# Optimization experiments

Hardware: AMD Instinct MI355X
Metric: run time of the kernel (lower is better)

## Reference

```python
import jax, jax.numpy as jnp
import numpy as np

CTX = 2048
D_IN = 2048
D_OUT = 2048
N_HEADS = 16
HEAD_DIM = D_OUT // N_HEADS
ROPE_BASE = 10000.0


def rope_tables(head_dim, ctx):
    inv_freq = 1.0 / (ROPE_BASE ** (jnp.arange(0, head_dim, 2, dtype=jnp.float32) / head_dim))
    angles = jnp.arange(ctx, dtype=jnp.float32)[:, None] * inv_freq[None, :]  # [ctx, hd/2]
    angles = jnp.concatenate([angles, angles], axis=1)  # [ctx, hd]
    return jnp.sin(angles), jnp.cos(angles)


def apply_rope(x, sin, cos):
    # x: [b, h, s, d]; rotate-by-half (Raschka / Llama style)
    s = x.shape[2]
    d = x.shape[3]
    x1, x2 = x[..., : d // 2], x[..., d // 2 :]
    rotated = jnp.concatenate([-x2, x1], axis=-1)
    return x * cos[:s][None, None] + rotated * sin[:s][None, None]


def setup_inputs() -> dict:
    key = jax.random.key(0)
    kx, kq, kk, kv, ko = jax.random.split(key, 5)
    scale = 0.02
    return {
        "x": jax.random.normal(kx, (2, CTX, D_IN), dtype=jnp.float32),
        "W_query": jax.random.normal(kq, (D_IN, D_OUT), dtype=jnp.float32) * scale,
        "W_key": jax.random.normal(kk, (D_IN, D_OUT), dtype=jnp.float32) * scale,
        "W_value": jax.random.normal(kv, (D_IN, D_OUT), dtype=jnp.float32) * scale,
        "W_out": jax.random.normal(ko, (D_OUT, D_OUT), dtype=jnp.float32) * scale,
    }


def reference(x, W_query, W_key, W_value, W_out):
    bs, cl, _ = x.shape
    sin, cos = rope_tables(HEAD_DIM, CTX)

    def split_heads(t):  # [b, s, d_out] -> [b, h, s, hd]
        return t.reshape(bs, cl, N_HEADS, HEAD_DIM).transpose(0, 2, 1, 3)

    q = split_heads(x @ W_query)
    k = split_heads(x @ W_key)
    v = split_heads(x @ W_value)

    q = apply_rope(q, sin, cos)
    k = apply_rope(k, sin, cos)

    # NOTE: original module does NOT scale by 1/sqrt(head_dim)
    scores = jnp.einsum("bhqd,bhkd->bhqk", q, k)
    causal = jnp.triu(jnp.ones((cl, cl), dtype=bool), k=1)
    scores = jnp.where(causal[None, None], -jnp.inf, scores)
    weights = jax.nn.softmax(scores, axis=-1)
    ctx = jnp.einsum("bhqk,bhkd->bhqd", weights, v)
    ctx = ctx.transpose(0, 2, 1, 3).reshape(bs, cl, N_HEADS * HEAD_DIM)
    return ctx @ W_out
```

## Files before the change

kernel.cpp:

```cpp
#include <hip/hip_runtime.h>
#include <cstdint>
#include <cstddef>

typedef _Float16 f16;
typedef _Float16 f16x8 __attribute__((ext_vector_type(8)));
typedef _Float16 f16x4 __attribute__((ext_vector_type(4)));
typedef float    f32x4 __attribute__((ext_vector_type(4)));
typedef float    f32x16 __attribute__((ext_vector_type(16)));
typedef int      i32x4 __attribute__((ext_vector_type(4)));

#define S_CTX 2048
#define NH 16
#define DH 128

#define BAR() asm volatile("s_barrier" ::: "memory")
#define VMW(n) asm volatile("s_waitcnt vmcnt(" #n ")" ::: "memory")
#define MF(a, b, c) __builtin_amdgcn_mfma_f32_16x16x32_f16((a), (b), (c), 0, 0, 0)
#define MF32(a, b, c) __builtin_amdgcn_mfma_f32_32x32x16_f16((a), (b), (c), 0, 0, 0)

__device__ __forceinline__ void gload16(const void* g, void* l) {
  __builtin_amdgcn_global_load_lds(
      (const __attribute__((address_space(1))) void*)g,
      (__attribute__((address_space(3))) void*)l, 16, 0, 0);
}

__device__ __forceinline__ int pk2(float a, float b) {
  auto hv = __builtin_amdgcn_cvt_pkrtz(a, b);
  return __builtin_bit_cast(int, hv);
}
__device__ __forceinline__ void pl_swap(int& a, int& b) {
  asm volatile("v_permlane32_swap_b32 %0, %1" : "+v"(a), "+v"(b));
}

__global__ void prep(const float* __restrict__ x,
                     const float* __restrict__ w0, const float* __restrict__ w1,
                     const float* __restrict__ w2, const float* __restrict__ w3,
                     f16* __restrict__ xb,
                     f16* __restrict__ o0, f16* __restrict__ o1,
                     f16* __restrict__ o2, f16* __restrict__ o3,
                     float* __restrict__ sint, float* __restrict__ cost) {
  const int bid = blockIdx.x, tid = threadIdx.x;
  if (bid < 512) {
    int idx = bid * 256 + tid;
    int j = idx & 63, s = idx >> 6;
    float invf = __expf(-(float)(2 * j) * (1.0f / 128.0f) * 9.210340371976184f);
    float a = (float)s * invf;
    sint[idx] = sinf(a);
    cost[idx] = cosf(a);
  } else if (bid < 8704) {
    int i = ((bid - 512) * 256 + tid) * 4;
    float4 v = *(const float4*)(x + i);
    f16x4 o; o[0] = (f16)v.x; o[1] = (f16)v.y; o[2] = (f16)v.z; o[3] = (f16)v.w;
    *(f16x4*)(xb + i) = o;
  } else {
    int b2 = bid - 8704;
    int z = b2 >> 12, rem = b2 & 4095;
    int by = rem >> 6, bx = rem & 63;
    int tx = tid & 31, ty = tid >> 5;
    const float* in; f16* out;
    switch (z) {
      case 0: in = w0; out = o0; break;
      case 1: in = w1; out = o1; break;
      case 2: in = w2; out = o2; break;
      default: in = w3; out = o3; break;
    }
    __shared__ float tl[32][33];
    int xc = bx * 32 + tx, yc = by * 32 + ty;
#pragma unroll
    for (int r = 0; r < 32; r += 8)
      tl[ty + r][tx] = in[(size_t)(yc + r) * 2048 + xc];
    __syncthreads();
    int xo = by * 32 + tx, yo = bx * 32 + ty;
#pragma unroll
    for (int r = 0; r < 32; r += 8)
      out[(size_t)(yo + r) * 2048 + xo] = (f16)tl[tx][ty + r];
  }
}

__global__ __launch_bounds__(512, 1)
void gemm_qk(const f16* __restrict__ A, const f16* __restrict__ wqT,
             const f16* __restrict__ wkT,
             f16* __restrict__ qb, f16* __restrict__ kb,
             const float* __restrict__ sint, const float* __restrict__ cost) {
  extern __shared__ __align__(16) char lds[];
  const int tid = threadIdx.x, lane = tid & 63;
  const int wvi = tid >> 6, wm = wvi >> 2, wn = wvi & 3;
  const int gcol = blockIdx.x * 256;
  const int proj = gcol >> 11;
  const int col0 = gcol & 2047;
  const int row0 = blockIdx.y * 256;
  const f16* Bt = proj ? wkT : wqT;

  const int ca0 = tid, ca1 = tid + 512;
  const int ra0 = ca0 >> 2, ra1 = ca1 >> 2;
  const int sa0 = (ca0 & 3) ^ ((ra0 >> 1) & 3);
  const int sa1 = (ca1 & 3) ^ ((ra1 >> 1) & 3);
  const f16* gA0 = A + (size_t)(row0 + ra0) * 2048 + sa0 * 8;
  const f16* gA1 = A + (size_t)(row0 + ra1) * 2048 + sa1 * 8;
  const f16* gB0 = Bt + (size_t)(col0 + ra0) * 2048 + sa0 * 8;
  const f16* gB1 = Bt + (size_t)(col0 + ra1) * 2048 + sa1 * 8;

  const int kslot = lane >> 4;
  int aoff[8], boff[4];
#pragma unroll
  for (int i = 0; i < 8; i++) {
    int row = wm * 128 + i * 16 + (lane & 15);
    aoff[i] = row * 64 + ((kslot ^ ((row >> 1) & 3)) << 4);
  }
#pragma unroll
  for (int j = 0; j < 4; j++) {
    int rb = (wn >> 1) * 128 + (wn & 1) * 32 + (j & 1) * 16 + (j >> 1) * 64 + (lane & 15);
    boff[j] = rb * 64 + ((kslot ^ ((rb >> 1) & 3)) << 4);
  }

  f32x4 acc[8][4] = {};

#define QKPH(SLOT, HS, SSLOT, DOSTAGE, WN) do {                                \
    const char* As_ = lds + (SLOT) * 32768;                                    \
    const char* Bs_ = As_ + 16384;                                             \
    f16x8 af[8], bf[4];                                                        \
    _Pragma("unroll") for (int i_ = 0; i_ < 8; i_++)                           \
      af[i_] = *(const f16x8*)(As_ + aoff[i_]);                                \
    _Pragma("unroll") for (int j_ = 0; j_ < 4; j_++)                           \
      bf[j_] = *(const f16x8*)(Bs_ + boff[j_]);                                \
    if (DOSTAGE) {                                                             \
      char* dA = lds + (SSLOT) * 32768;                                        \
      gload16(gA0 + (HS) * 32, dA + ca0 * 16);                                 \
      gload16(gA1 + (HS) * 32, dA + ca1 * 16);                                 \
      gload16(gB0 + (HS) * 32, dA + 16384 + ca0 * 16);                         \
      gload16(gB1 + (HS) * 32, dA + 16384 + ca1 * 16);                         \
    }                                                                          \
    asm volatile("s_waitcnt vmcnt(" #WN ")" ::: "memory");                     \
    BAR();                                                                     \
    __builtin_amdgcn_s_setprio(1);                                             \
    _Pragma("unroll") for (int i_ = 0; i_ < 8; i_++)                           \
      _Pragma("unroll") for (int j_ = 0; j_ < 4; j_++)                         \
        acc[i_][j_] = MF(af[i_], bf[j_], acc[i_][j_]);                         \
    __builtin_amdgcn_s_setprio(0);                                             \
    BAR();                                                                     \
  } while (0)

#pragma unroll
  for (int h = 0; h < 2; h++) {
    char* dA = lds + h * 32768;
    gload16(gA0 + h * 32, dA + ca0 * 16);
    gload16(gA1 + h * 32, dA + ca1 * 16);
    gload16(gB0 + h * 32, dA + 16384 + ca0 * 16);
    gload16(gB1 + h * 32, dA + 16384 + ca1 * 16);
  }
  VMW(4); BAR();

  for (int t = 0; t < 20; ++t) {
    const int hb = 3 * t;
    QKPH(0, hb + 2, 2, 1, 4);
    QKPH(1, hb + 3, 0, 1, 4);
    QKPH(2, hb + 4, 1, 1, 4);
  }
  QKPH(0, 62, 2, 1, 4);
  QKPH(1, 63, 0, 1, 4);
  QKPH(2, 0, 0, 0, 0);
  QKPH(0, 0, 0, 0, 63);
#undef QKPH

  const int b = row0 >> 11, sb = row0 & 2047;
  f16* dst = proj ? kb : qb;
  const int h = (col0 >> 7) + (wn >> 1);
#pragma unroll
  for (int i = 0; i < 8; i++)
#pragma unroll
    for (int jj = 0; jj < 2; jj++)
#pragma unroll
      for (int r = 0; r < 4; r++) {
        int s = sb + wm * 128 + i * 16 + (lane >> 4) * 4 + r;
        int d = (wn & 1) * 32 + jj * 16 + (lane & 15);
        float cv = cost[s * 64 + d], sv = sint[s * 64 + d];
        float x1 = acc[i][jj][r], x2 = acc[i][jj + 2][r];
        size_t base = ((size_t)(b * NH + h) * S_CTX + s) << 7;
        dst[base + d]      = (f16)(x1 * cv - x2 * sv);
        dst[base + d + 64] = (f16)(x2 * cv + x1 * sv);
      }
}

template<int MODE>
__global__ __launch_bounds__(512, 1)
void gemm8(const f16* __restrict__ A, const f16* __restrict__ Bt,
           f16* __restrict__ vtb, float* __restrict__ of) {
  extern __shared__ __align__(16) char lds[];
#define RING_A(e) (lds + (e) * 16384)
#define RING_B(e) (lds + 65536 + (e) * 8192)
  const int tid = threadIdx.x, lane = tid & 63;
  const int wvi = tid >> 6, wm = wvi >> 1, wn = wvi & 1;
  const int col0 = blockIdx.x * 128;
  const int row0 = blockIdx.y * 256;

  const int ca0 = tid, ca1 = tid + 512, cb0 = tid;
  const int rAs0 = ca0 >> 2, rAs1 = ca1 >> 2, rBs0 = cb0 >> 2;
  const int sA0 = (ca0 & 3) ^ ((rAs0 >> 1) & 3);
  const int sA1 = (ca1 & 3) ^ ((rAs1 >> 1) & 3);
  const int sB0 = (cb0 & 3) ^ ((rBs0 >> 1) & 3);
  const f16* gA0 = A + (size_t)(row0 + rAs0) * 2048 + sA0 * 8;
  const f16* gA1 = A + (size_t)(row0 + rAs1) * 2048 + sA1 * 8;
  const f16* gB0 = Bt + (size_t)(col0 + rBs0) * 2048 + sB0 * 8;

  const int kslot = lane >> 4;
  int aoff[4], boff[4];
#pragma unroll
  for (int i = 0; i < 4; i++) {
    int row = wm * 64 + i * 16 + (lane & 15);
    aoff[i] = row * 64 + ((kslot ^ ((row >> 1) & 3)) << 4);
  }
#pragma unroll
  for (int j = 0; j < 4; j++) {
    int rb = wn * 32 + (j & 1) * 16 + (j >> 1) * 64 + (lane & 15);
    boff[j] = rb * 64 + ((kslot ^ ((rb >> 1) & 3)) << 4);
  }

  f32x4 acc[4][4] = {};

#define PH8(SLOT, HS, DOSTAGE, WN) do {                                        \
    const char* As_ = RING_A(SLOT);                                            \
    const char* Bs_ = RING_B(SLOT);                                            \
    f16x8 af[4], bf[4];                                                        \
    _Pragma("unroll") for (int i_ = 0; i_ < 4; i_++)                           \
      af[i_] = *(const f16x8*)(As_ + aoff[i_]);                                \
    _Pragma("unroll") for (int j_ = 0; j_ < 4; j_++)                           \
      bf[j_] = *(const f16x8*)(Bs_ + boff[j_]);                                \
    if (DOSTAGE) {                                                             \
      gload16(gA0 + (HS) * 32, RING_A((HS) & 3) + ca0 * 16);                   \
      gload16(gA1 + (HS) * 32, RING_A((HS) & 3) + ca1 * 16);                   \
      gload16(gB0 + (HS) * 32, RING_B((HS) & 3) + cb0 * 16);                   \
    }                                                                          \
    asm volatile("s_waitcnt vmcnt(" #WN ")" ::: "memory");                     \
    BAR();                                                                     \
    __builtin_amdgcn_s_setprio(1);                                             \
    _Pragma("unroll") for (int i_ = 0; i_ < 4; i_++)                           \
      _Pragma("unroll") for (int j_ = 0; j_ < 4; j_++)                         \
        acc[i_][j_] = MF(af[i_], bf[j_], acc[i_][j_]);                         \
    __builtin_amdgcn_s_setprio(0);                                             \
    BAR();                                                                     \
  } while (0)

#pragma unroll
  for (int h = 0; h < 3; h++) {
    gload16(gA0 + h * 32, RING_A(h) + ca0 * 16);
    gload16(gA1 + h * 32, RING_A(h) + ca1 * 16);
    gload16(gB0 + h * 32, RING_B(h) + cb0 * 16);
  }
  VMW(6); BAR();

  for (int t = 0; t < 15; ++t) {
    const int p = t * 4;
    PH8(0, p + 3, 1, 6);
    PH8(1, p + 4, 1, 6);
    PH8(2, p + 5, 1, 6);
    PH8(3, p + 6, 1, 6);
  }
  PH8(0, 63, 1, 6);
  PH8(1, 0, 0, 3);
  PH8(2, 0, 0, 0);
  PH8(3, 0, 0, 63);
#undef PH8

  const int b = row0 >> 11, sbase = row0 & 2047;

  if (MODE == 2) {
#pragma unroll
    for (int i = 0; i < 4; i++)
#pragma unroll
      for (int j = 0; j < 4; j++)
#pragma unroll
        for (int r = 0; r < 4; r++) {
          int row = row0 + wm * 64 + i * 16 + (lane >> 4) * 4 + r;
          int col = col0 + wn * 32 + (j & 1) * 16 + (j >> 1) * 64 + (lane & 15);
          of[(size_t)row * 2048 + col] = acc[i][j][r];
        }
  } else {
    const int h = col0 >> 7;
    f16x4* ldsv = (f16x4*)lds;
#pragma unroll
    for (int i = 0; i < 4; i++)
#pragma unroll
      for (int j = 0; j < 4; j++) {
        f16x4 v;
#pragma unroll
        for (int r = 0; r < 4; r++) v[r] = (f16)acc[i][j][r];
        int su = wm * 16 + i * 4 + (lane >> 4);
        int d  = wn * 32 + (j & 1) * 16 + (j >> 1) * 64 + (lane & 15);
        ldsv[d * 64 + (su ^ ((d << 1) & 63))] = v;
      }
    __syncthreads();
#pragma unroll
    for (int it = 0; it < 8; ++it) {
      int o = it * 512 + tid;
      int d = o >> 5, c = o & 31;
      int xc = (d << 1) & 63;
      f16x4 lo = ldsv[d * 64 + ((2 * c) ^ xc)];
      f16x4 hi = ldsv[d * 64 + ((2 * c + 1) ^ xc)];
      f16x8 vv;
      vv[0] = lo[0]; vv[1] = lo[1]; vv[2] = lo[2]; vv[3] = lo[3];
      vv[4] = hi[0]; vv[5] = hi[1]; vv[6] = hi[2]; vv[7] = hi[3];
      *(f16x8*)&vtb[((size_t)(b * NH + h) * DH + d) * S_CTX + sbase + c * 8] = vv;
    }
  }
#undef RING_A
#undef RING_B
}

__global__ __launch_bounds__(512, 1)
void attn_k(const f16* __restrict__ q, const f16* __restrict__ kk,
            const f16* __restrict__ vt, f16* __restrict__ ctx) {
  extern __shared__ __align__(16) char alds[];
  const int tid = threadIdx.x, lane = tid & 63;
  const int halfid = tid >> 8;
  const int tid2 = tid & 255;
  const int wv2 = tid2 >> 6;
  const int lh = lane >> 5, q31 = lane & 31;
  const int bid = blockIdx.x;
  const int bh = (bid & 7) + 8 * ((bid >> 3) & 3);
  const int idxQ = bid >> 5;
  const int b = bh >> 4, h = bh & 15;
  const size_t plane = (size_t)bh * (S_CTX * DH);
  const f16* Qp = q + plane;
  const f16* Kp = kk + plane;
  const f16* Vp = vt + plane;
  const float LOG2E = 1.4426950408889634f;

  char* myH = alds + halfid * 65536;
  float* O_lds = (float*)(alds + 65536);
  float* ml_lds = (float*)alds;

#define STAGE(T, BUF) do {                                                      \
    const f16* Kt = Kp + (size_t)(T) * 64 * DH;                                 \
    const f16* Vt = Vp + (size_t)(T) * 64;                                      \
    char* kb_ = myH + (BUF) * 16384;                                            \
    char* vb_ = myH + 32768 + (BUF) * 16384;                                    \
    _Pragma("unroll") for (int j_ = 0; j_ < 4; j_++) {                          \
      int c = tid2 + j_ * 256; int rk = c >> 4;                                 \
      gload16(Kt + (size_t)rk * DH + (((c & 15) ^ (rk & 7)) * 8), kb_ + c * 16); \
    }                                                                           \
    _Pragma("unroll") for (int j_ = 0; j_ < 4; j_++) {                          \
      int c = tid2 + j_ * 256; int rv = c >> 3;                                 \
      gload16(Vt + (size_t)rv * S_CTX + (((c & 7) ^ (rv & 7)) * 8), vb_ + c * 16); \
    }                                                                           \
  } while (0)

  for (int p = 0; p < 2; ++p) {
    const int Qt = p ? (15 - idxQ) : idxQ;
    const int q0 = Qt * 128;
    const int NTh = Qt + 1;

    f16x8 qf[8];
    {
      const f16* qq = Qp + (size_t)(q0 + wv2 * 32 + q31) * DH + lh * 8;
#pragma unroll
      for (int s = 0; s < 8; s++) {
        qf[s] = *(const f16x8*)(qq + s * 16);
#pragma unroll
        for (int e = 0; e < 8; e++) qf[s][e] = (f16)((float)qf[s][e] * LOG2E);
      }
    }
    float m_ = -3e38f, l_ = 0.f;
    f32x16 o[4] = {};

    STAGE(halfid, 0);
    VMW(0); BAR();

    int cur = 0;
    for (int i = 0; i < NTh; i++) {
      const int t = 2 * i + halfid;
      if (i + 1 < NTh) STAGE(2 * (i + 1) + halfid, cur ^ 1);
      const f16* Ksc = (const f16*)(myH + cur * 16384);
      const f16* Vsc = (const f16*)(myH + 32768 + cur * 16384);

      f32x16 st0 = {}, st1 = {};
      __builtin_amdgcn_s_setprio(1);
#pragma unroll
      for (int s = 0; s < 8; s++) {
        const int r0 = q31, r1 = 32 + q31;
        f16x8 kf0 = *(const f16x8*)&Ksc[r0 * 128 + (((2 * s + lh) ^ (r0 & 7)) << 3)];
        f16x8 kf1 = *(const f16x8*)&Ksc[r1 * 128 + (((2 * s + lh) ^ (r1 & 7)) << 3)];
        st0 = MF32(kf0, qf[s], st0);
        st1 = MF32(kf1, qf[s], st1);
      }
      __builtin_amdgcn_s_setprio(0);

      if (t >= 2 * Qt) {
        const int qg = q0 + wv2 * 32 + q31;
#pragma unroll
        for (int r = 0; r < 16; r++) {
          int kvb = t * 64 + (r & 3) + 8 * (r >> 2) + 4 * lh;
          if (kvb > qg) st0[r] = -3e38f;
          if (kvb + 32 > qg) st1[r] = -3e38f;
        }
      }
      float mx = st0[0];
#pragma unroll
      for (int r = 1; r < 16; r++) mx = fmaxf(mx, st0[r]);
#pragma unroll
      for (int r = 0; r < 16; r++) mx = fmaxf(mx, st1[r]);
      mx = fmaxf(mx, __shfl_xor(mx, 32));
      if (__any(mx > m_ + 8.0f)) {
        float nm = fmaxf(m_, mx);
        float al = __builtin_amdgcn_exp2f(m_ - nm);
        m_ = nm; l_ *= al;
#pragma unroll
        for (int r = 0; r < 16; r++) {
          float alr = __shfl(al, (r & 3) + 8 * (r >> 2) + 4 * lh);
#pragma unroll
          for (int j = 0; j < 4; j++) o[j][r] *= alr;
        }
      }
      float s_ = 0.f;
#pragma unroll
      for (int r = 0; r < 16; r++) { st0[r] = __builtin_amdgcn_exp2f(st0[r] - m_); s_ += st0[r]; }
#pragma unroll
      for (int r = 0; r < 16; r++) { st1[r] = __builtin_amdgcn_exp2f(st1[r] - m_); s_ += st1[r]; }
      s_ += __shfl_xor(s_, 32);
      l_ += s_;

      f16x8 pa[4];
      {
        int w0 = pk2(st0[0], st0[1]),   w1 = pk2(st0[2], st0[3]);
        int w2 = pk2(st0[4], st0[5]),   w3 = pk2(st0[6], st0[7]);
        int w4 = pk2(st0[8], st0[9]),   w5 = pk2(st0[10], st0[11]);
        int w6 = pk2(st0[12], st0[13]), w7 = pk2(st0[14], st0[15]);
        pl_swap(w0, w2); pl_swap(w1, w3); pl_swap(w4, w6); pl_swap(w5, w7);
        i32x4 a = {w0, w1, w2, w3}; pa[0] = __builtin_bit_cast(f16x8, a);
        i32x4 bb = {w4, w5, w6, w7}; pa[1] = __builtin_bit_cast(f16x8, bb);
      }
      {
        int w0 = pk2(st1[0], st1[1]),   w1 = pk2(st1[2], st1[3]);
        int w2 = pk2(st1[4], st1[5]),   w3 = pk2(st1[6], st1[7]);
        int w4 = pk2(st1[8], st1[9]),   w5 = pk2(st1[10], st1[11]);
        int w6 = pk2(st1[12], st1[13]), w7 = pk2(st1[14], st1[15]);
        pl_swap(w0, w2); pl_swap(w1, w3); pl_swap(w4, w6); pl_swap(w5, w7);
        i32x4 a = {w0, w1, w2, w3}; pa[2] = __builtin_bit_cast(f16x8, a);
        i32x4 bb = {w4, w5, w6, w7}; pa[3] = __builtin_bit_cast(f16x8, bb);
      }

      __builtin_amdgcn_s_setprio(1);
#pragma unroll
      for (int j = 0; j < 4; j++) {
        const int rv = 32 * j + q31;
#pragma unroll
        for (int s2 = 0; s2 < 4; s2++) {
          f16x8 vf = *(const f16x8*)&Vsc[rv * 64 + (((2 * s2 + lh) ^ (rv & 7)) << 3)];
          o[j] = MF32(pa[s2], vf, o[j]);
        }
      }
      __builtin_amdgcn_s_setprio(0);

      VMW(0); BAR();
      cur ^= 1;
    }

    if (halfid) {
      ml_lds[(wv2 * 32 + q31) * 2]     = m_;
      ml_lds[(wv2 * 32 + q31) * 2 + 1] = l_;
#pragma unroll
      for (int r = 0; r < 16; r++) {
        int crow = (r & 3) + 8 * (r >> 2) + 4 * lh;
#pragma unroll
        for (int j = 0; j < 4; j++)
          O_lds[(wv2 * 32 + crow) * 128 + 32 * j + q31] = o[j][r];
      }
    }
    BAR();
    if (!halfid) {
      float mB = ml_lds[(wv2 * 32 + q31) * 2];
      float lB = ml_lds[(wv2 * 32 + q31) * 2 + 1];
      float m = fmaxf(m_, mB);
      float aA = __builtin_amdgcn_exp2f(m_ - m);
      float aB = __builtin_amdgcn_exp2f(mB - m);
      float lfin = l_ * aA + lB * aB;
      float inv = 1.0f / lfin;
#pragma unroll
      for (int r = 0; r < 16; r++) {
        int crow = (r & 3) + 8 * (r >> 2) + 4 * lh;
        float aAr = __shfl(aA, crow);
        float aBr = __shfl(aB, crow);
        float invr = __shfl(inv, crow);
        int qg = q0 + wv2 * 32 + crow;
#pragma unroll
        for (int j = 0; j < 4; j++) {
          float ov = o[j][r] * aAr + O_lds[(wv2 * 32 + crow) * 128 + 32 * j + q31] * aBr;
          ctx[((size_t)(b * S_CTX + qg) * 2048) + h * 128 + 32 * j + q31] = (f16)(ov * invr);
        }
      }
    }
    BAR();
  }
#undef STAGE
}

extern "C" void kernel_launch(void* const* d_in, const int* in_sizes, int n_in,
                              void* d_out, int out_size, void* d_ws, size_t ws_size,
                              hipStream_t stream) {
  (void)in_sizes; (void)n_in; (void)out_size; (void)ws_size;
  const float* x  = (const float*)d_in[0];
  const float* Wq = (const float*)d_in[1];
  const float* Wk = (const float*)d_in[2];
  const float* Wv = (const float*)d_in[3];
  const float* Wo = (const float*)d_in[4];
  float* out = (float*)d_out;
  char* ws = (char*)d_ws;

  f16*   xb   = (f16*)(ws);
  f16*   ctxb = (f16*)(ws);
  f16*   wqT  = (f16*)(ws + 16777216);
  f16*   wkT  = (f16*)(ws + 25165824);
  f16*   wvT  = (f16*)(ws + 33554432);
  f16*   woT  = (f16*)(ws + 41943040);
  f16*   qb   = (f16*)(ws + 50331648);
  f16*   kb   = (f16*)(ws + 67108864);
  f16*   vtb  = (f16*)(ws + 83886080);
  float* sint = (float*)(ws + 100663296);
  float* cost = (float*)(ws + 101187584);

  prep<<<dim3(25088), dim3(256), 0, stream>>>(x, Wq, Wk, Wv, Wo, xb,
                                              wqT, wkT, wvT, woT, sint, cost);
  gemm_qk<<<dim3(16, 16), dim3(512), 98304, stream>>>(xb, wqT, wkT, qb, kb, sint, cost);
  gemm8<1><<<dim3(16, 16), dim3(512), 98304, stream>>>(xb, wvT, vtb, nullptr);
  attn_k<<<dim3(256), dim3(512), 131072, stream>>>(qb, kb, vtb, ctxb);
  gemm8<2><<<dim3(16, 16), dim3(512), 98304, stream>>>(ctxb, woT, nullptr, out);
}
```

Baseline: 242.2 us.

## Prefetch A fragments into double-buffered registers and deepen the QK LDS ring

Both projection GEMMs now stage the next k-step's A fragments from LDS into a second register set while the MFMAs for the current step run. This hides LDS read latency behind matrix math. gemm_qk also moves from a 3-slot to a 4-slot LDS ring, which raises its dynamic LDS to 128 KB, and both kernels declare launch bounds of two blocks per CU. The LDS sizes likely still allow only one block per CU, so the tighter register budget mainly adds risk. gemm_qk already holds 128 accumulator registers and now keeps two fragment sets, so it may spill.

```diff
diff --git a/kernel.cpp b/kernel.cpp
--- a/kernel.cpp
+++ b/kernel.cpp
@@ -77,7 +77,7 @@
   }
 }
 
-__global__ __launch_bounds__(512, 1)
+__global__ __launch_bounds__(512, 2)
 void gemm_qk(const f16* __restrict__ A, const f16* __restrict__ wqT,
              const f16* __restrict__ wkT,
              f16* __restrict__ qb, f16* __restrict__ kb,
@@ -114,53 +114,59 @@
   }
 
   f32x4 acc[8][4] = {};
-
-#define QKPH(SLOT, HS, SSLOT, DOSTAGE, WN) do {                                \
-    const char* As_ = lds + (SLOT) * 32768;                                    \
-    const char* Bs_ = As_ + 16384;                                             \
-    f16x8 af[8], bf[4];                                                        \
+  f16x8 afA[8], afB[8];
+
+#define QKSTG(H) do {                                                          \
+    char* d_ = lds + ((H) & 3) * 32768;                                        \
+    gload16(gA0 + (H) * 32, d_ + ca0 * 16);                                    \
+    gload16(gA1 + (H) * 32, d_ + ca1 * 16);                                    \
+    gload16(gB0 + (H) * 32, d_ + 16384 + ca0 * 16);                            \
+    gload16(gB1 + (H) * 32, d_ + 16384 + ca1 * 16);                            \
+  } while (0)
+
+#define RDAF(DST, S)                                                           \
     _Pragma("unroll") for (int i_ = 0; i_ < 8; i_++)                           \
-      af[i_] = *(const f16x8*)(As_ + aoff[i_]);                                \
-    _Pragma("unroll") for (int j_ = 0; j_ < 4; j_++)                           \
-      bf[j_] = *(const f16x8*)(Bs_ + boff[j_]);                                \
-    if (DOSTAGE) {                                                             \
-      char* dA = lds + (SSLOT) * 32768;                                        \
-      gload16(gA0 + (HS) * 32, dA + ca0 * 16);                                 \
-      gload16(gA1 + (HS) * 32, dA + ca1 * 16);                                 \
-      gload16(gB0 + (HS) * 32, dA + 16384 + ca0 * 16);                         \
-      gload16(gB1 + (HS) * 32, dA + 16384 + ca1 * 16);                         \
-    }                                                                          \
-    asm volatile("s_waitcnt vmcnt(" #WN ")" ::: "memory");                     \
-    BAR();                                                                     \
+      DST[i_] = *(const f16x8*)(lds + (S) * 32768 + aoff[i_])
+
+#define MFMC(AF, BFR) do {                                                     \
     __builtin_amdgcn_s_setprio(1);                                             \
     _Pragma("unroll") for (int i_ = 0; i_ < 8; i_++)                           \
       _Pragma("unroll") for (int j_ = 0; j_ < 4; j_++)                         \
-        acc[i_][j_] = MF(af[i_], bf[j_], acc[i_][j_]);                         \
+        acc[i_][j_] = MF(AF[i_], BFR[j_], acc[i_][j_]);                        \
     __builtin_amdgcn_s_setprio(0);                                             \
+  } while (0)
+
+#define QKP(CUR, NXT, SBF, SNX, HSTG, DOSTAGE, PREF, WN) do {                  \
+    if (DOSTAGE) QKSTG(HSTG);                                                  \
+    asm volatile("s_waitcnt vmcnt(" #WN ")" ::: "memory");                     \
+    BAR();                                                                     \
+    f16x8 bf[4];                                                               \
+    _Pragma("unroll") for (int j_ = 0; j_ < 4; j_++)                           \
+      bf[j_] = *(const f16x8*)(lds + (SBF) * 32768 + 16384 + boff[j_]);        \
+    if (PREF) { RDAF(NXT, SNX); }                                              \
+    MFMC(CUR, bf);                                                             \
     BAR();                                                                     \
   } while (0)
 
-#pragma unroll
-  for (int h = 0; h < 2; h++) {
-    char* dA = lds + h * 32768;
-    gload16(gA0 + h * 32, dA + ca0 * 16);
-    gload16(gA1 + h * 32, dA + ca1 * 16);
-    gload16(gB0 + h * 32, dA + 16384 + ca0 * 16);
-    gload16(gB1 + h * 32, dA + 16384 + ca1 * 16);
-  }
-  VMW(4); BAR();
-
-  for (int t = 0; t < 20; ++t) {
-    const int hb = 3 * t;
-    QKPH(0, hb + 2, 2, 1, 4);
-    QKPH(1, hb + 3, 0, 1, 4);
-    QKPH(2, hb + 4, 1, 1, 4);
-  }
-  QKPH(0, 62, 2, 1, 4);
-  QKPH(1, 63, 0, 1, 4);
-  QKPH(2, 0, 0, 0, 0);
-  QKPH(0, 0, 0, 0, 63);
-#undef QKPH
+  QKSTG(0); QKSTG(1); QKSTG(2);
+  VMW(8); BAR();
+  RDAF(afA, 0);
+
+  for (int t = 0; t < 15; ++t) {
+    const int hb = 4 * t;
+    QKP(afA, afB, 0, 1, hb + 3, 1, 1, 8);
+    QKP(afB, afA, 1, 2, hb + 4, 1, 1, 8);
+    QKP(afA, afB, 2, 3, hb + 5, 1, 1, 8);
+    QKP(afB, afA, 3, 0, hb + 6, 1, 1, 8);
+  }
+  QKP(afA, afB, 0, 1, 63, 1, 1, 8);
+  QKP(afB, afA, 1, 2, 0, 0, 1, 4);
+  QKP(afA, afB, 2, 3, 0, 0, 1, 0);
+  QKP(afB, afA, 3, 0, 0, 0, 0, 0);
+#undef QKP
+#undef MFMC
+#undef RDAF
+#undef QKSTG
 
   const int b = row0 >> 11, sb = row0 & 2047;
   f16* dst = proj ? kb : qb;
@@ -182,7 +188,7 @@
 }
 
 template<int MODE>
-__global__ __launch_bounds__(512, 1)
+__global__ __launch_bounds__(512, 2)
 void gemm8(const f16* __restrict__ A, const f16* __restrict__ Bt,
            f16* __restrict__ vtb, float* __restrict__ of) {
   extern __shared__ __align__(16) char lds[];
@@ -216,50 +222,52 @@
   }
 
   f32x4 acc[4][4] = {};
-
-#define PH8(SLOT, HS, DOSTAGE, WN) do {                                        \
-    const char* As_ = RING_A(SLOT);                                            \
-    const char* Bs_ = RING_B(SLOT);                                            \
-    f16x8 af[4], bf[4];                                                        \
+  f16x8 afA[4], afB[4];
+
+#define G8STG(H) do {                                                          \
+    gload16(gA0 + (H) * 32, RING_A((H) & 3) + ca0 * 16);                       \
+    gload16(gA1 + (H) * 32, RING_A((H) & 3) + ca1 * 16);                       \
+    gload16(gB0 + (H) * 32, RING_B((H) & 3) + cb0 * 16);                       \
+  } while (0)
+
+#define G8RDAF(DST, S)                                                         \
     _Pragma("unroll") for (int i_ = 0; i_ < 4; i_++)                           \
-      af[i_] = *(const f16x8*)(As_ + aoff[i_]);                                \
-    _Pragma("unroll") for (int j_ = 0; j_ < 4; j_++)                           \
-      bf[j_] = *(const f16x8*)(Bs_ + boff[j_]);                                \
-    if (DOSTAGE) {                                                             \
-      gload16(gA0 + (HS) * 32, RING_A((HS) & 3) + ca0 * 16);                   \
-      gload16(gA1 + (HS) * 32, RING_A((HS) & 3) + ca1 * 16);                   \
-      gload16(gB0 + (HS) * 32, RING_B((HS) & 3) + cb0 * 16);                   \
-    }                                                                          \
+      DST[i_] = *(const f16x8*)(RING_A(S) + aoff[i_])
+
+#define G8P(CUR, NXT, SBF, SNX, HSTG, DOSTAGE, PREF, WN) do {                  \
+    if (DOSTAGE) G8STG(HSTG);                                                  \
     asm volatile("s_waitcnt vmcnt(" #WN ")" ::: "memory");                     \
     BAR();                                                                     \
+    f16x8 bf[4];                                                               \
+    _Pragma("unroll") for (int j_ = 0; j_ < 4; j_++)                           \
+      bf[j_] = *(const f16x8*)(RING_B(SBF) + boff[j_]);                        \
+    if (PREF) { G8RDAF(NXT, SNX); }                                            \
     __builtin_amdgcn_s_setprio(1);                                             \
     _Pragma("unroll") for (int i_ = 0; i_ < 4; i_++)                           \
       _Pragma("unroll") for (int j_ = 0; j_ < 4; j_++)                         \
-        acc[i_][j_] = MF(af[i_], bf[j_], acc[i_][j_]);                         \
+        acc[i_][j_] = MF(CUR[i_], bf[j_], acc[i_][j_]);                        \
     __builtin_amdgcn_s_setprio(0);                                             \
     BAR();                                                                     \
   } while (0)
 
-#pragma unroll
-  for (int h = 0; h < 3; h++) {
-    gload16(gA0 + h * 32, RING_A(h) + ca0 * 16);
-    gload16(gA1 + h * 32, RING_A(h) + ca1 * 16);
-    gload16(gB0 + h * 32, RING_B(h) + cb0 * 16);
-  }
+  G8STG(0); G8STG(1); G8STG(2);
   VMW(6); BAR();
+  G8RDAF(afA, 0);
 
   for (int t = 0; t < 15; ++t) {
-    const int p = t * 4;
-    PH8(0, p + 3, 1, 6);
-    PH8(1, p + 4, 1, 6);
-    PH8(2, p + 5, 1, 6);
-    PH8(3, p + 6, 1, 6);
-  }
-  PH8(0, 63, 1, 6);
-  PH8(1, 0, 0, 3);
-  PH8(2, 0, 0, 0);
-  PH8(3, 0, 0, 63);
-#undef PH8
+    const int hb = 4 * t;
+    G8P(afA, afB, 0, 1, hb + 3, 1, 1, 6);
+    G8P(afB, afA, 1, 2, hb + 4, 1, 1, 6);
+    G8P(afA, afB, 2, 3, hb + 5, 1, 1, 6);
+    G8P(afB, afA, 3, 0, hb + 6, 1, 1, 6);
+  }
+  G8P(afA, afB, 0, 1, 63, 1, 1, 6);
+  G8P(afB, afA, 1, 2, 0, 0, 1, 3);
+  G8P(afA, afB, 2, 3, 0, 0, 1, 0);
+  G8P(afB, afA, 3, 0, 0, 0, 0, 0);
+#undef G8P
+#undef G8RDAF
+#undef G8STG
 
   const int b = row0 >> 11, sbase = row0 & 2047;
 
@@ -519,7 +527,7 @@
 
   prep<<<dim3(25088), dim3(256), 0, stream>>>(x, Wq, Wk, Wv, Wo, xb,
                                               wqT, wkT, wvT, woT, sint, cost);
-  gemm_qk<<<dim3(16, 16), dim3(512), 98304, stream>>>(xb, wqT, wkT, qb, kb, sint, cost);
+  gemm_qk<<<dim3(16, 16), dim3(512), 131072, stream>>>(xb, wqT, wkT, qb, kb, sint, cost);
   gemm8<1><<<dim3(16, 16), dim3(512), 98304, stream>>>(xb, wvT, vtb, nullptr);
   attn_k<<<dim3(256), dim3(512), 131072, stream>>>(qb, kb, vtb, ctxb);
   gemm8<2><<<dim3(16, 16), dim3(512), 98304, stream>>>(ctxb, woT, nullptr, out);
```

Measured after the change: 286.0 us. 18.1% more time.
